# Performance work log

Hardware: AMD Instinct MI355X
Metric: run time of the kernel (lower is better)

## Reference

```python
import jax, jax.numpy as jnp
import numpy as np

N_NODES = 100000
N_EDGES = 3200000
N_GRAPHS = 1024
F_IN = 78
H = 128
BN_EPS = 1e-5


def setup_inputs() -> dict:
    key = jax.random.key(0)
    ks = jax.random.split(key, 10)
    x = jax.random.normal(ks[0], (N_NODES, F_IN), dtype=jnp.float32)
    edge_index = jax.random.randint(ks[1], (2, N_EDGES), 0, N_NODES, dtype=jnp.int64)
    batch = jnp.sort(jax.random.randint(ks[2], (N_NODES,), 0, N_GRAPHS, dtype=jnp.int64))
    s_in = 1.0 / np.sqrt(F_IN)
    s_h = 1.0 / np.sqrt(H)
    return {
        "x": x,
        "edge_index": edge_index,
        "batch": batch,
        "W1_0": jax.random.normal(ks[3], (F_IN, H), dtype=jnp.float32) * s_in,
        "b1_0": jnp.zeros((H,), jnp.float32),
        "W2_0": jax.random.normal(ks[4], (H, H), dtype=jnp.float32) * s_h,
        "b2_0": jnp.zeros((H,), jnp.float32),
        "W1": jax.random.normal(ks[5], (4, H, H), dtype=jnp.float32) * s_h,
        "b1": jnp.zeros((4, H), jnp.float32),
        "W2": jax.random.normal(ks[6], (4, H, H), dtype=jnp.float32) * s_h,
        "b2": jnp.zeros((4, H), jnp.float32),
        "gamma": jnp.ones((5, H), jnp.float32),
        "beta": jnp.zeros((5, H), jnp.float32),
        "Wf": jax.random.normal(ks[7], (2 * H, H), dtype=jnp.float32) * (1.0 / np.sqrt(2 * H)),
        "bf": jnp.zeros((H,), jnp.float32),
    }


def _gin_layer(x, src, dst, W1l, b1l, W2l, b2l, g, bta):
    # GINConv, eps=0: h_i = x_i + sum_{(j->i) in E} x_j, then 2-layer MLP
    agg = jax.ops.segment_sum(x[src], dst, num_segments=N_NODES)  # [N, F]
    h = x + agg
    h = jax.nn.relu(h @ W1l + b1l) @ W2l + b2l
    h = jax.nn.relu(h)
    # BatchNorm1d (training mode: biased batch statistics)
    mu = jnp.mean(h, axis=0)
    var = jnp.mean(jnp.square(h - mu), axis=0)
    return (h - mu) * (g / jnp.sqrt(var + BN_EPS)) + bta


def reference(x, edge_index, batch, W1_0, b1_0, W2_0, b2_0, W1, b1, W2, b2, gamma, beta, Wf, bf):
    src, dst = edge_index[0], edge_index[1]
    # layer 0 (no residual: dims 78 -> 128)
    h = _gin_layer(x, src, dst, W1_0, b1_0, W2_0, b2_0, gamma[0], beta[0])
    # layers 1..4 with residual
    for i in range(4):
        h_new = _gin_layer(h, src, dst, W1[i], b1[i], W2[i], b2[i], gamma[i + 1], beta[i + 1])
        h = h + h_new
    # global mean pool
    sums = jax.ops.segment_sum(h, batch, num_segments=N_GRAPHS)  # [G, H]
    counts = jax.ops.segment_sum(jnp.ones((h.shape[0],), h.dtype), batch, num_segments=N_GRAPHS)
    mean_pool = sums / jnp.maximum(counts, 1.0)[:, None]
    # global max pool (empty segments -> 0)
    max_pool = jax.ops.segment_max(h, batch, num_segments=N_GRAPHS)
    max_pool = jnp.where(counts[:, None] > 0, max_pool, 0.0)
    combined = jnp.concatenate([mean_pool, max_pool], axis=1)  # [G, 2H]
    return combined @ Wf + bf
```

## Files before the change

### kernel.cpp

```cpp
#include <hip/hip_runtime.h>
#include <float.h>

#define N_NODES 100000
#define N_EDGES 3200000
#define N_GRAPHS 1024
#define F_IN 78
#define H 128
#define BN_EPS 1e-5f

#define BK_SHIFT 7
#define BK_NODES 128
#define NBUCKETS ((N_NODES + BK_NODES - 1) / BK_NODES)

#define P3_BLOCKS 800
#define P3_CHUNK 4000

using short8 = __attribute__((ext_vector_type(8))) short;
using f32x4v = __attribute__((ext_vector_type(4))) float;

__device__ __forceinline__ unsigned short f2bf(float f) {
    unsigned int u = __float_as_uint(f);
    unsigned int r = (u + 0x7fffu + ((u >> 16) & 1u)) >> 16;
    return (unsigned short)r;
}
__device__ __forceinline__ float bf_lo(unsigned int u) { return __uint_as_float(u << 16); }
__device__ __forceinline__ float bf_hi(unsigned int u) { return __uint_as_float(u & 0xffff0000u); }
__device__ __forceinline__ float bf1(unsigned short u) { return __uint_as_float((unsigned int)u << 16); }


__global__ __launch_bounds__(256) void k_hist(const int* __restrict__ dst,
                                              int* __restrict__ bofs) {
    __shared__ int lcnt[NBUCKETS];
    for (int i = threadIdx.x; i < NBUCKETS; i += 256) lcnt[i] = 0;
    __syncthreads();
    int base = blockIdx.x * P3_CHUNK;
    for (int j = threadIdx.x; j < P3_CHUNK; j += 256)
        atomicAdd(&lcnt[dst[base + j] >> BK_SHIFT], 1);
    __syncthreads();
    for (int i = threadIdx.x; i < NBUCKETS; i += 256)
        bofs[blockIdx.x * NBUCKETS + i] = lcnt[i];
}

__global__ __launch_bounds__(256) void k_scan_a(int* __restrict__ bofs,
                                                int* __restrict__ btot) {
    __shared__ int part[256];
    int b = blockIdx.x, t = threadIdx.x;
    int val[4];
#pragma unroll
    for (int j = 0; j < 4; ++j) {
        int idx = t * 4 + j;
        val[j] = (idx < P3_BLOCKS) ? bofs[idx * NBUCKETS + b] : 0;
    }
    part[t] = val[0] + val[1] + val[2] + val[3];
    __syncthreads();
    if (t == 0) {
        int run = 0;
        for (int u = 0; u < 256; ++u) { int tmp = part[u]; part[u] = run; run += tmp; }
        btot[b] = run;
    }
    __syncthreads();
    int off = part[t];
#pragma unroll
    for (int j = 0; j < 4; ++j) {
        int idx = t * 4 + j;
        if (idx < P3_BLOCKS) {
            int tmp = val[j];
            bofs[idx * NBUCKETS + b] = off;
            off += tmp;
        }
    }
}

__global__ __launch_bounds__(1024) void k_scan_b(const int* __restrict__ btot,
                                                 int* __restrict__ bbase,
                                                 int* __restrict__ row_start) {
    __shared__ int tot[1024];
    int t = threadIdx.x;
    tot[t] = (t < NBUCKETS) ? btot[t] : 0;
    __syncthreads();
    if (t == 0) {
        int acc = 0;
        for (int i = 0; i < NBUCKETS; ++i) { int v = tot[i]; tot[i] = acc; acc += v; }
    }
    __syncthreads();
    if (t < NBUCKETS) bbase[t] = tot[t];
    if (t == 0) {
        bbase[NBUCKETS] = N_EDGES;
        row_start[N_NODES] = N_EDGES;
    }
}

__global__ __launch_bounds__(256) void k_p3b(const int* __restrict__ src,
                                             const int* __restrict__ dst,
                                             const int* __restrict__ bofs,
                                             const int* __restrict__ bbase,
                                             unsigned int* __restrict__ ebuf) {
    __shared__ int cur[NBUCKETS];
    for (int i = threadIdx.x; i < NBUCKETS; i += 256)
        cur[i] = bbase[i] + bofs[blockIdx.x * NBUCKETS + i];
    __syncthreads();
    int base = blockIdx.x * P3_CHUNK;
    for (int j = threadIdx.x; j < P3_CHUNK; j += 256) {
        int d = dst[base + j];
        int p = atomicAdd(&cur[d >> BK_SHIFT], 1);
        ebuf[p] = ((unsigned int)src[base + j] << 7) | (unsigned int)(d & (BK_NODES - 1));
    }
}

__global__ __launch_bounds__(256) void k_p4(const int* __restrict__ bbase,
                                            const unsigned int* __restrict__ ebuf,
                                            int* __restrict__ esrc,
                                            int* __restrict__ row_start) {
    __shared__ int cur[BK_NODES];
    __shared__ int start[BK_NODES];
    int b = blockIdx.x;
    int nodeBase = b << BK_SHIFT;
    int nLocal = min(BK_NODES, N_NODES - nodeBase);
    if (threadIdx.x < BK_NODES) cur[threadIdx.x] = 0;
    __syncthreads();
    int s = bbase[b], e = bbase[b + 1];
    for (int p = s + threadIdx.x; p < e; p += 256)
        atomicAdd(&cur[ebuf[p] & (BK_NODES - 1)], 1);
    __syncthreads();
    if (threadIdx.x == 0) {
        int run = s;
        for (int i = 0; i < nLocal; ++i) { start[i] = run; run += cur[i]; }
    }
    __syncthreads();
    if (threadIdx.x < nLocal) {
        row_start[nodeBase + threadIdx.x] = start[threadIdx.x];
        cur[threadIdx.x] = start[threadIdx.x];
    }
    __syncthreads();
    for (int p = s + threadIdx.x; p < e; p += 256) {
        unsigned int ed = ebuf[p];
        int q = atomicAdd(&cur[ed & (BK_NODES - 1)], 1);
        esrc[q] = (int)(ed >> 7);
    }
}


__global__ void k_cast_x(const float* __restrict__ x, unsigned short* __restrict__ xb) {
    int i = blockIdx.x * blockDim.x + threadIdx.x;
    if (i >= N_NODES * 96) return;
    int node = i / 96;
    int c = i - node * 96;
    float v = (c < F_IN) ? x[(size_t)node * F_IN + c] : 0.f;
    xb[i] = f2bf(v);
}

__global__ void k_cast_w(const float* __restrict__ W2_0, const float* __restrict__ W1,
                         const float* __restrict__ W2, unsigned short* __restrict__ Wt) {
    int i = blockIdx.x * blockDim.x + threadIdx.x;
    if (i >= 9 * H * H) return;
    int w = i >> 14, r = i & 16383;
    int n = r >> 7, k = r & 127;
    const float* s = (w == 0) ? W2_0 : (w <= 4 ? W1 + (w - 1) * H * H : W2 + (w - 5) * H * H);
    Wt[i] = f2bf(s[k * H + n]);
}

__global__ void k_cast_w0(const float* __restrict__ W1_0, unsigned short* __restrict__ Wt0) {
    int i = blockIdx.x * blockDim.x + threadIdx.x;
    if (i >= H * 96) return;
    int n = i / 96, k = i - n * 96;
    Wt0[i] = f2bf((k < F_IN) ? W1_0[k * H + n] : 0.f);
}


__global__ void k_gather96(const unsigned int* __restrict__ xw,
                           const int* __restrict__ row_start, const int* __restrict__ esrc,
                           unsigned int* __restrict__ out) {
    int wave = threadIdx.x >> 6;
    int lane = threadIdx.x & 63;
    int node = blockIdx.x * 4 + wave;
    int s = row_start[node], e = row_start[node + 1];
    bool act = lane < 48;
    unsigned int su = act ? xw[node * 48 + lane] : 0u;
    float aA[8], aB[8];
#pragma unroll
    for (int j = 0; j < 8; ++j) { aA[j] = 0.f; aB[j] = 0.f; }
    aA[0] = bf_lo(su); aB[0] = bf_hi(su);
    int p = s;
    for (; p + 16 <= e; p += 16) {
        int idx[16];
#pragma unroll
        for (int j = 0; j < 16; ++j) idx[j] = esrc[p + j];
        unsigned int u[16];
#pragma unroll
        for (int j = 0; j < 16; ++j) u[j] = act ? xw[idx[j] * 48 + lane] : 0u;
#pragma unroll
        for (int j = 0; j < 16; ++j) { aA[j & 7] += bf_lo(u[j]); aB[j & 7] += bf_hi(u[j]); }
    }
    for (; p + 4 <= e; p += 4) {
        int i0 = esrc[p], i1 = esrc[p + 1], i2 = esrc[p + 2], i3 = esrc[p + 3];
        unsigned int u0 = act ? xw[i0 * 48 + lane] : 0u;
        unsigned int u1 = act ? xw[i1 * 48 + lane] : 0u;
        unsigned int u2 = act ? xw[i2 * 48 + lane] : 0u;
        unsigned int u3 = act ? xw[i3 * 48 + lane] : 0u;
        aA[0] += bf_lo(u0); aB[0] += bf_hi(u0); aA[1] += bf_lo(u1); aB[1] += bf_hi(u1);
        aA[2] += bf_lo(u2); aB[2] += bf_hi(u2); aA[3] += bf_lo(u3); aB[3] += bf_hi(u3);
    }
    for (; p < e; ++p) {
        unsigned int u = act ? xw[esrc[p] * 48 + lane] : 0u;
        aA[0] += bf_lo(u); aB[0] += bf_hi(u);
    }
    if (act) {
        float rx = ((aA[0] + aA[1]) + (aA[2] + aA[3])) + ((aA[4] + aA[5]) + (aA[6] + aA[7]));
        float ry = ((aB[0] + aB[1]) + (aB[2] + aB[3])) + ((aB[4] + aB[5]) + (aB[6] + aB[7]));
        out[node * 48 + lane] = (unsigned int)f2bf(rx) | ((unsigned int)f2bf(ry) << 16);
    }
}

__global__ void k_gather128b(const unsigned int* __restrict__ hw,
                             const int* __restrict__ row_start, const int* __restrict__ esrc,
                             unsigned int* __restrict__ aggb) {
    int wave = threadIdx.x >> 6;
    int lane = threadIdx.x & 63;
    int node = blockIdx.x * 4 + wave;
    int s = row_start[node], e = row_start[node + 1];
    unsigned int su = hw[node * 64 + lane];
    float aA[8], aB[8];
#pragma unroll
    for (int j = 0; j < 8; ++j) { aA[j] = 0.f; aB[j] = 0.f; }
    aA[0] = bf_lo(su); aB[0] = bf_hi(su);
    int p = s;
    for (; p + 16 <= e; p += 16) {
        int idx[16];
#pragma unroll
        for (int j = 0; j < 16; ++j) idx[j] = esrc[p + j];
        unsigned int u[16];
#pragma unroll
        for (int j = 0; j < 16; ++j) u[j] = hw[idx[j] * 64 + lane];
#pragma unroll
        for (int j = 0; j < 16; ++j) { aA[j & 7] += bf_lo(u[j]); aB[j & 7] += bf_hi(u[j]); }
    }
    for (; p + 4 <= e; p += 4) {
        int i0 = esrc[p], i1 = esrc[p + 1], i2 = esrc[p + 2], i3 = esrc[p + 3];
        unsigned int u0 = hw[i0 * 64 + lane];
        unsigned int u1 = hw[i1 * 64 + lane];
        unsigned int u2 = hw[i2 * 64 + lane];
        unsigned int u3 = hw[i3 * 64 + lane];
        aA[0] += bf_lo(u0); aB[0] += bf_hi(u0); aA[1] += bf_lo(u1); aB[1] += bf_hi(u1);
        aA[2] += bf_lo(u2); aB[2] += bf_hi(u2); aA[3] += bf_lo(u3); aB[3] += bf_hi(u3);
    }
    for (; p < e; ++p) {
        unsigned int u = hw[esrc[p] * 64 + lane];
        aA[0] += bf_lo(u); aB[0] += bf_hi(u);
    }
    float rx = ((aA[0] + aA[1]) + (aA[2] + aA[3])) + ((aA[4] + aA[5]) + (aA[6] + aA[7]));
    float ry = ((aB[0] + aB[1]) + (aB[2] + aB[3])) + ((aB[4] + aB[5]) + (aB[6] + aB[7]));
    aggb[node * 64 + lane] = (unsigned int)f2bf(rx) | ((unsigned int)f2bf(ry) << 16);
}


template <int NK1>
__global__ __launch_bounds__(256) void k_mlp(const short* __restrict__ A,
                                             const short* __restrict__ Wt1,
                                             const float* __restrict__ b1v,
                                             const short* __restrict__ Wt2,
                                             const float* __restrict__ b2v,
                                             unsigned short* __restrict__ out,
                                             float* __restrict__ gsum,
                                             float* __restrict__ gss) {
    const int K1 = NK1 * 32;
    __shared__ unsigned short act1[64 * H];
    __shared__ float lsum[H], lss[H];
    if (threadIdx.x < H) { lsum[threadIdx.x] = 0.f; lss[threadIdx.x] = 0.f; }
    int wave = threadIdx.x >> 6, lane = threadIdx.x & 63;
    int r0 = blockIdx.x * 64 + wave * 16;
    int lm = lane & 15, lk = lane >> 4;
    int arow = r0 + lm;
    if (arow >= N_NODES) arow = N_NODES - 1;
    const short8* Arow = (const short8*)(A + (size_t)arow * K1);
    f32x4v acc[8];
#pragma unroll
    for (int n = 0; n < 8; ++n) {
        float bv = b1v[n * 16 + lm];
        acc[n] = (f32x4v){bv, bv, bv, bv};
    }
#pragma unroll
    for (int ks = 0; ks < NK1; ++ks) {
        short8 af = Arow[ks * 4 + lk];
#pragma unroll
        for (int n = 0; n < 8; ++n) {
            const short8* Brow = (const short8*)(Wt1 + (size_t)(n * 16 + lm) * K1);
            short8 bfr = Brow[ks * 4 + lk];
            acc[n] = __builtin_amdgcn_mfma_f32_16x16x32_bf16(af, bfr, acc[n], 0, 0, 0);
        }
    }
#pragma unroll
    for (int n = 0; n < 8; ++n) {
        int colb = (n * 16 + lm) * 2;
#pragma unroll
        for (int rg = 0; rg < 4; ++rg) {
            int rl = wave * 16 + lk * 4 + rg;
            int byte = (rl * 256 + colb) ^ ((rl & 7) << 4);
            *(unsigned short*)((char*)act1 + byte) = f2bf(fmaxf(acc[n][rg], 0.f));
        }
    }
    __syncthreads();
    f32x4v acc2[8];
#pragma unroll
    for (int n = 0; n < 8; ++n) {
        float bv = b2v[n * 16 + lm];
        acc2[n] = (f32x4v){bv, bv, bv, bv};
    }
    int rlr = wave * 16 + lm;
#pragma unroll
    for (int ks = 0; ks < 4; ++ks) {
        int byte = (rlr * 256 + ks * 64 + lk * 16) ^ ((rlr & 7) << 4);
        short8 af = *(const short8*)((char*)act1 + byte);
#pragma unroll
        for (int n = 0; n < 8; ++n) {
            const short8* Brow = (const short8*)(Wt2 + (size_t)(n * 16 + lm) * H);
            short8 bfr = Brow[ks * 4 + lk];
            acc2[n] = __builtin_amdgcn_mfma_f32_16x16x32_bf16(af, bfr, acc2[n], 0, 0, 0);
        }
    }
#pragma unroll
    for (int n = 0; n < 8; ++n) {
        int col = n * 16 + lm;
        float s = 0.f, q = 0.f;
#pragma unroll
        for (int rg = 0; rg < 4; ++rg) {
            int r = r0 + lk * 4 + rg;
            if (r < N_NODES) {
                float v = fmaxf(acc2[n][rg], 0.f);
                out[(size_t)r * H + col] = f2bf(v);
                s += v;
                q += v * v;
            }
        }
        atomicAdd(&lsum[col], s);
        atomicAdd(&lss[col], q);
    }
    __syncthreads();
    if (threadIdx.x < H) {
        atomicAdd(&gsum[threadIdx.x], lsum[threadIdx.x]);
        atomicAdd(&gss[threadIdx.x], lss[threadIdx.x]);
    }
}


__global__ void k_bnfinal(float* __restrict__ gsum, float* __restrict__ gss,
                          const float* __restrict__ gamma, const float* __restrict__ beta,
                          float* __restrict__ scale, float* __restrict__ shift) {
    int c = threadIdx.x;
    const float inv_n = 1.f / (float)N_NODES;
    float sv = gsum[c], qv = gss[c];
    gsum[c] = 0.f;
    gss[c] = 0.f;
    float mu = sv * inv_n;
    float var = fmaxf(qv * inv_n - mu * mu, 0.f);
    float sc = gamma[c] * rsqrtf(var + BN_EPS);
    scale[c] = sc;
    shift[c] = beta[c] - mu * sc;
}

template <bool RES, bool WB>
__global__ void k_bnapply(const uint2* __restrict__ vb, const float* __restrict__ scale,
                          const float* __restrict__ shift, float* __restrict__ h,
                          uint2* __restrict__ hb) {
    int idx = blockIdx.x * blockDim.x + threadIdx.x;
    if (idx >= N_NODES * H / 4) return;
    int c4 = idx & 31;
    uint2 pv = vb[idx];
    float4 val = make_float4(bf_lo(pv.x), bf_hi(pv.x), bf_lo(pv.y), bf_hi(pv.y));
    float4 sc = reinterpret_cast<const float4*>(scale)[c4];
    float4 sh = reinterpret_cast<const float4*>(shift)[c4];
    float4 r;
    r.x = val.x * sc.x + sh.x;
    r.y = val.y * sc.y + sh.y;
    r.z = val.z * sc.z + sh.z;
    r.w = val.w * sc.w + sh.w;
    if (RES) {
        float4 hv = reinterpret_cast<float4*>(h)[idx];
        r.x += hv.x; r.y += hv.y; r.z += hv.z; r.w += hv.w;
    }
    reinterpret_cast<float4*>(h)[idx] = r;
    if (WB) {
        uint2 pk;
        pk.x = (unsigned int)f2bf(r.x) | ((unsigned int)f2bf(r.y) << 16);
        pk.y = (unsigned int)f2bf(r.z) | ((unsigned int)f2bf(r.w) << 16);
        hb[idx] = pk;
    }
}


__global__ void k_bounds(const int* __restrict__ batch, int* __restrict__ row_begin) {
    int i = blockIdx.x * blockDim.x + threadIdx.x;
    if (i >= N_NODES) return;
    int bi = batch[i];
    int bp = (i == 0) ? -1 : batch[i - 1];
    for (int g = bp + 1; g <= bi; ++g) row_begin[g] = i;
    if (i == N_NODES - 1) {
        for (int g = bi + 1; g <= N_GRAPHS; ++g) row_begin[g] = N_NODES;
    }
}

__global__ void k_pool_f(const unsigned short* __restrict__ act, const float* __restrict__ scale,
                         const float* __restrict__ shift, const float* __restrict__ h3,
                         const int* __restrict__ row_begin, float* __restrict__ pooled) {
    int g = blockIdx.x;
    int c = threadIdx.x;
    float sc = scale[c], sh = shift[c];
    int s = row_begin[g], e = row_begin[g + 1];
    float sum = 0.f, mx = -FLT_MAX;
    for (int i = s; i < e; ++i) {
        float v = h3[(size_t)i * H + c] + sc * bf1(act[(size_t)i * H + c]) + sh;
        sum += v;
        mx = fmaxf(mx, v);
    }
    int cnt = e - s;
    pooled[g * 256 + c]       = (cnt > 0) ? sum / (float)cnt : 0.f;
    pooled[g * 256 + 128 + c] = (cnt > 0) ? mx : 0.f;
}

__global__ void k_final(const float* __restrict__ pooled, const float* __restrict__ Wf,
                        const float* __restrict__ bf, float* __restrict__ out) {
    __shared__ float ps[256];
    int g = blockIdx.x, c = threadIdx.x;
    ps[c] = pooled[g * 256 + c];
    ps[128 + c] = pooled[g * 256 + 128 + c];
    __syncthreads();
    float acc = bf[c];
#pragma unroll 8
    for (int k = 0; k < 256; ++k) acc += ps[k] * Wf[k * H + c];
    out[g * H + c] = acc;
}


extern "C" void kernel_launch(void* const* d_in, const int* in_sizes, int n_in,
                              void* d_out, int out_size, void* d_ws, size_t ws_size,
                              hipStream_t stream) {
    const float* x     = (const float*)d_in[0];
    const int*   ei    = (const int*)d_in[1];
    const int*   src   = ei;
    const int*   dst   = ei + N_EDGES;
    const int*   batch = (const int*)d_in[2];
    const float* W1_0  = (const float*)d_in[3];
    const float* b1_0  = (const float*)d_in[4];
    const float* W2_0  = (const float*)d_in[5];
    const float* b2_0  = (const float*)d_in[6];
    const float* W1    = (const float*)d_in[7];
    const float* b1    = (const float*)d_in[8];
    const float* W2    = (const float*)d_in[9];
    const float* b2    = (const float*)d_in[10];
    const float* gamma = (const float*)d_in[11];
    const float* beta  = (const float*)d_in[12];
    const float* Wf    = (const float*)d_in[13];
    const float* bf    = (const float*)d_in[14];
    float* out = (float*)d_out;

    char* ws = (char*)d_ws;
    size_t off = 0;
    auto alloc = [&](size_t bytes) -> void* {
        void* p = ws + off;
        off = (off + bytes + 255) & ~(size_t)255;
        return p;
    };

    float* h    = (float*)alloc((size_t)N_NODES * H * 4);
    uint2* hb   = (uint2*)alloc((size_t)N_NODES * H * 2);
    unsigned int*   aggb  = (unsigned int*)alloc((size_t)N_NODES * H * 2);
    unsigned short* act2b = (unsigned short*)alloc((size_t)N_NODES * H * 2);
    unsigned short* xb    = (unsigned short*)alloc((size_t)N_NODES * 96 * 2);
    unsigned int*   agg0b = (unsigned int*)alloc((size_t)N_NODES * 48 * 4);
    unsigned short* Wtall = (unsigned short*)alloc((size_t)9 * H * H * 2);
    unsigned short* Wt0   = (unsigned short*)alloc((size_t)H * 96 * 2);
    int* row_start = (int*)alloc((size_t)(N_NODES + 1) * 4);
    int* esrc      = (int*)alloc((size_t)N_EDGES * 4);
    unsigned int* ebuf = (unsigned int*)alloc((size_t)N_EDGES * 4);
    int* bofs      = (int*)alloc((size_t)P3_BLOCKS * NBUCKETS * 4);
    int* btot      = (int*)alloc((size_t)NBUCKETS * 4);
    int* bbase     = (int*)alloc((size_t)(NBUCKETS + 1) * 4);
    float* gsum  = (float*)alloc(H * 4);
    float* gss   = (float*)alloc(H * 4);
    float* scale = (float*)alloc(H * 4);
    float* shift = (float*)alloc(H * 4);
    int* row_begin = (int*)alloc((size_t)(N_GRAPHS + 1) * 4);
    float* pooled  = (float*)alloc((size_t)N_GRAPHS * 256 * 4);

    k_cast_x<<<(N_NODES * 96 + 255) / 256, 256, 0, stream>>>(x, xb);
    k_cast_w<<<(9 * H * H + 255) / 256, 256, 0, stream>>>(W2_0, W1, W2, Wtall);
    k_cast_w0<<<(H * 96 + 255) / 256, 256, 0, stream>>>(W1_0, Wt0);

    k_hist<<<P3_BLOCKS, 256, 0, stream>>>(dst, bofs);
    k_scan_a<<<NBUCKETS, 256, 0, stream>>>(bofs, btot);
    k_scan_b<<<1, 1024, 0, stream>>>(btot, bbase, row_start);
    k_p3b<<<P3_BLOCKS, 256, 0, stream>>>(src, dst, bofs, bbase, ebuf);
    k_p4<<<NBUCKETS, 256, 0, stream>>>(bbase, ebuf, esrc, row_start);

    hipMemsetAsync(gsum, 0, H * 4, stream);
    hipMemsetAsync(gss, 0, H * 4, stream);

    const int mfma_grid = (N_NODES + 63) / 64;

    k_gather96<<<N_NODES / 4, 256, 0, stream>>>((const unsigned int*)xb, row_start, esrc, agg0b);
    k_mlp<3><<<mfma_grid, 256, 0, stream>>>((const short*)agg0b, (const short*)Wt0, b1_0,
                                            (const short*)Wtall, b2_0, act2b, gsum, gss);
    k_bnfinal<<<1, 128, 0, stream>>>(gsum, gss, gamma, beta, scale, shift);
    k_bnapply<false, true><<<N_NODES * H / 4 / 256, 256, 0, stream>>>((const uint2*)act2b,
                                                                      scale, shift, h, hb);

    for (int l = 0; l < 4; ++l) {
        k_gather128b<<<N_NODES / 4, 256, 0, stream>>>((const unsigned int*)hb, row_start,
                                                      esrc, aggb);
        k_mlp<4><<<mfma_grid, 256, 0, stream>>>((const short*)aggb,
                                                (const short*)(Wtall + (1 + l) * H * H),
                                                b1 + l * H,
                                                (const short*)(Wtall + (5 + l) * H * H),
                                                b2 + l * H, act2b, gsum, gss);
        k_bnfinal<<<1, 128, 0, stream>>>(gsum, gss, gamma + (l + 1) * H, beta + (l + 1) * H,
                                         scale, shift);
        if (l < 3) {
            k_bnapply<true, true><<<N_NODES * H / 4 / 256, 256, 0, stream>>>((const uint2*)act2b,
                                                                             scale, shift, h, hb);
        }
    }

    k_bounds<<<(N_NODES + 255) / 256, 256, 0, stream>>>(batch, row_begin);
    k_pool_f<<<N_GRAPHS, 128, 0, stream>>>(act2b, scale, shift, h, row_begin, pooled);
    k_final<<<N_GRAPHS, 128, 0, stream>>>(pooled, Wf, bf, out);
}
```

Baseline: 1.272 ms.

## Drop fp32 residual buffer, keep residual stream in bf16; shrink edge-sort block count

```diff
diff --git a/kernel.cpp b/kernel.cpp
--- a/kernel.cpp
+++ b/kernel.cpp
@@ -12,8 +12,8 @@
 #define BK_NODES 128
 #define NBUCKETS ((N_NODES + BK_NODES - 1) / BK_NODES)
 
-#define P3_BLOCKS 800
-#define P3_CHUNK 4000
+#define P3_BLOCKS 200
+#define P3_CHUNK 16000
 
 using short8 = __attribute__((ext_vector_type(8))) short;
 using f32x4v = __attribute__((ext_vector_type(4))) float;
@@ -45,30 +45,16 @@
                                                 int* __restrict__ btot) {
     __shared__ int part[256];
     int b = blockIdx.x, t = threadIdx.x;
-    int val[4];
-#pragma unroll
-    for (int j = 0; j < 4; ++j) {
-        int idx = t * 4 + j;
-        val[j] = (idx < P3_BLOCKS) ? bofs[idx * NBUCKETS + b] : 0;
-    }
-    part[t] = val[0] + val[1] + val[2] + val[3];
+    int val = (t < P3_BLOCKS) ? bofs[t * NBUCKETS + b] : 0;
+    part[t] = val;
     __syncthreads();
     if (t == 0) {
         int run = 0;
-        for (int u = 0; u < 256; ++u) { int tmp = part[u]; part[u] = run; run += tmp; }
+        for (int u = 0; u < P3_BLOCKS; ++u) { int tmp = part[u]; part[u] = run; run += tmp; }
         btot[b] = run;
     }
     __syncthreads();
-    int off = part[t];
-#pragma unroll
-    for (int j = 0; j < 4; ++j) {
-        int idx = t * 4 + j;
-        if (idx < P3_BLOCKS) {
-            int tmp = val[j];
-            bofs[idx * NBUCKETS + b] = off;
-            off += tmp;
-        }
-    }
+    if (t < P3_BLOCKS) bofs[t * NBUCKETS + b] = part[t];
 }
 
 __global__ __launch_bounds__(1024) void k_scan_b(const int* __restrict__ btot,
@@ -357,10 +343,9 @@
     shift[c] = beta[c] - mu * sc;
 }
 
-template <bool RES, bool WB>
+template <bool RES>
 __global__ void k_bnapply(const uint2* __restrict__ vb, const float* __restrict__ scale,
-                          const float* __restrict__ shift, float* __restrict__ h,
-                          uint2* __restrict__ hb) {
+                          const float* __restrict__ shift, uint2* __restrict__ hb) {
     int idx = blockIdx.x * blockDim.x + threadIdx.x;
     if (idx >= N_NODES * H / 4) return;
     int c4 = idx & 31;
@@ -374,16 +359,13 @@
     r.z = val.z * sc.z + sh.z;
     r.w = val.w * sc.w + sh.w;
     if (RES) {
-        float4 hv = reinterpret_cast<float4*>(h)[idx];
-        r.x += hv.x; r.y += hv.y; r.z += hv.z; r.w += hv.w;
-    }
-    reinterpret_cast<float4*>(h)[idx] = r;
-    if (WB) {
-        uint2 pk;
-        pk.x = (unsigned int)f2bf(r.x) | ((unsigned int)f2bf(r.y) << 16);
-        pk.y = (unsigned int)f2bf(r.z) | ((unsigned int)f2bf(r.w) << 16);
-        hb[idx] = pk;
-    }
+        uint2 hv = hb[idx];
+        r.x += bf_lo(hv.x); r.y += bf_hi(hv.x); r.z += bf_lo(hv.y); r.w += bf_hi(hv.y);
+    }
+    uint2 pk;
+    pk.x = (unsigned int)f2bf(r.x) | ((unsigned int)f2bf(r.y) << 16);
+    pk.y = (unsigned int)f2bf(r.z) | ((unsigned int)f2bf(r.w) << 16);
+    hb[idx] = pk;
 }
 
 
@@ -399,7 +381,7 @@
 }
 
 __global__ void k_pool_f(const unsigned short* __restrict__ act, const float* __restrict__ scale,
-                         const float* __restrict__ shift, const float* __restrict__ h3,
+                         const float* __restrict__ shift, const unsigned short* __restrict__ hb3,
                          const int* __restrict__ row_begin, float* __restrict__ pooled) {
     int g = blockIdx.x;
     int c = threadIdx.x;
@@ -407,7 +389,7 @@
     int s = row_begin[g], e = row_begin[g + 1];
     float sum = 0.f, mx = -FLT_MAX;
     for (int i = s; i < e; ++i) {
-        float v = h3[(size_t)i * H + c] + sc * bf1(act[(size_t)i * H + c]) + sh;
+        float v = bf1(hb3[(size_t)i * H + c]) + sc * bf1(act[(size_t)i * H + c]) + sh;
         sum += v;
         mx = fmaxf(mx, v);
     }
@@ -460,7 +442,6 @@
         return p;
     };
 
-    float* h    = (float*)alloc((size_t)N_NODES * H * 4);
     uint2* hb   = (uint2*)alloc((size_t)N_NODES * H * 2);
     unsigned int*   aggb  = (unsigned int*)alloc((size_t)N_NODES * H * 2);
     unsigned short* act2b = (unsigned short*)alloc((size_t)N_NODES * H * 2);
@@ -500,8 +481,8 @@
     k_mlp<3><<<mfma_grid, 256, 0, stream>>>((const short*)agg0b, (const short*)Wt0, b1_0,
                                             (const short*)Wtall, b2_0, act2b, gsum, gss);
     k_bnfinal<<<1, 128, 0, stream>>>(gsum, gss, gamma, beta, scale, shift);
-    k_bnapply<false, true><<<N_NODES * H / 4 / 256, 256, 0, stream>>>((const uint2*)act2b,
-                                                                      scale, shift, h, hb);
+    k_bnapply<false><<<N_NODES * H / 4 / 256, 256, 0, stream>>>((const uint2*)act2b,
+                                                                scale, shift, hb);
 
     for (int l = 0; l < 4; ++l) {
         k_gather128b<<<N_NODES / 4, 256, 0, stream>>>((const unsigned int*)hb, row_start,
@@ -514,12 +495,13 @@
         k_bnfinal<<<1, 128, 0, stream>>>(gsum, gss, gamma + (l + 1) * H, beta + (l + 1) * H,
                                          scale, shift);
         if (l < 3) {
-            k_bnapply<true, true><<<N_NODES * H / 4 / 256, 256, 0, stream>>>((const uint2*)act2b,
-                                                                             scale, shift, h, hb);
+            k_bnapply<true><<<N_NODES * H / 4 / 256, 256, 0, stream>>>((const uint2*)act2b,
+                                                                       scale, shift, hb);
         }
     }
 
     k_bounds<<<(N_NODES + 255) / 256, 256, 0, stream>>>(batch, row_begin);
-    k_pool_f<<<N_GRAPHS, 128, 0, stream>>>(act2b, scale, shift, h, row_begin, pooled);
+    k_pool_f<<<N_GRAPHS, 128, 0, stream>>>(act2b, scale, shift,
+                                           (const unsigned short*)hb, row_begin, pooled);
     k_final<<<N_GRAPHS, 128, 0, stream>>>(pooled, Wf, bf, out);
 }
```

Measured after the change: 1.241 ms. 1.02x faster.
